# Performance work log

Hardware: AMD Instinct MI355X
Metric: run time of the kernel (lower is better)

Reference implementation:

```python
import jax, jax.numpy as jnp
import numpy as np

# --- quantization-format simulation helpers (numpy, used only in setup) ---
FP4_GRID = np.array([0.0, 0.5, 1.0, 1.5, 2.0, 3.0, 4.0, 6.0], np.float32)  # e2m1 magnitudes
FP4_MID = (FP4_GRID[:-1] + FP4_GRID[1:]) / 2.0
E4M3_MAX = 448.0


def _round_e4m3(x):
    """Round-to-nearest onto an fp8 e4m3-like grid (3 mantissa bits, clamp to 448)."""
    x = np.clip(x, -E4M3_MAX, E4M3_MAX)
    a = np.abs(x)
    e = np.clip(np.floor(np.log2(np.maximum(a, 1e-12))), -6, 8)
    step = np.exp2(e - 3)
    return (np.round(x / step) * step).astype(np.float32)


def _quant_fp4_mag(a):
    """Nearest e2m1 magnitude for non-negative a."""
    idx = np.searchsorted(FP4_MID, a)
    return FP4_GRID[idx]


def setup_inputs() -> dict:
    rng = np.random.default_rng(0)
    IN, OUT, P = 4096, 4096, 8
    k_fp8 = ((IN // P + 127) // 128) * 128   # 512
    k_fp4 = IN - k_fp8                       # 3584

    w = (rng.standard_normal((OUT, IN)) * 0.023).astype(np.float32)
    w4 = w[:, :k_fp4]
    w8 = w[:, k_fp4:]

    # --- NVFP4 quantization: per-128 fp32 outer scale, per-16 e4m3 inner scale ---
    b128 = w4.reshape(OUT, k_fp4 // 128, 128)
    os = np.maximum(np.abs(b128).max(-1) / (6.0 * E4M3_MAX), 1e-12).astype(np.float32)  # (OUT, k4/128)
    b16 = w4.reshape(OUT, k_fp4 // 128, 8, 16)
    is_q = _round_e4m3(np.abs(b16).max(-1) / 6.0 / os[..., None])  # (OUT, k4/128, 8)
    denom = np.maximum(is_q * os[..., None], 1e-12)
    q4 = np.sign(b16) * _quant_fp4_mag(np.abs(b16) / denom[..., None])
    w_q_fp4 = q4.reshape(OUT, k_fp4).astype(np.float32)
    w_is_fp4 = is_q.reshape(OUT, k_fp4 // 16).astype(np.float32)
    w_os_fp4 = os

    # --- fp8 quantization: per-32 e8m0 (power-of-2) scale ---
    b32 = w8.reshape(OUT, k_fp8 // 32, 32)
    amax = np.maximum(np.abs(b32).max(-1), 1e-12)
    s8 = np.exp2(np.ceil(np.log2(amax / E4M3_MAX))).astype(np.float32)
    w_q_fp8 = _round_e4m3(b32 / s8[..., None]).reshape(OUT, k_fp8)
    w_s_fp8 = s8

    # --- dequantized transposed weight buffer (as the module precomputes) ---
    w4_dq = w_q_fp4 * np.repeat(w_is_fp4, 16, 1) * np.repeat(w_os_fp4, 128, 1)
    w8_dq = w_q_fp8 * np.repeat(w_s_fp8, 32, 1)
    w_t = np.ascontiguousarray(np.concatenate([w4_dq, w8_dq], 1).T)  # (IN, OUT)

    x = rng.standard_normal((8192, IN)).astype(np.float32)
    return {
        "x": jnp.asarray(x),
        "w_q_fp4": jnp.asarray(w_q_fp4),
        "w_os_fp4": jnp.asarray(w_os_fp4),
        "w_is_fp4": jnp.asarray(w_is_fp4),
        "w_t": jnp.asarray(w_t),
        "w_q_fp8": jnp.asarray(w_q_fp8),
        "w_s_fp8": jnp.asarray(w_s_fp8),
    }


def reference(x, w_q_fp4, w_os_fp4, w_is_fp4, w_t, w_q_fp8, w_s_fp8):
    OUT = w_q_fp4.shape[0]
    k4 = w_q_fp4.shape[1]
    # fused dequant of fp4 partition: value * inner_scale(per 16) * outer_scale(per 128)
    w4 = (w_q_fp4.reshape(OUT, k4 // 16, 16) * w_is_fp4[..., None]).reshape(OUT, k4)
    w4 = (w4.reshape(OUT, k4 // 128, 128) * w_os_fp4[..., None]).reshape(OUT, k4)
    # dequant of fp8 partition: value * e8m0 scale (per 32)
    k8 = w_q_fp8.shape[1]
    w8 = (w_q_fp8.reshape(OUT, k8 // 32, 32) * w_s_fp8[..., None]).reshape(OUT, k8)
    W = jnp.concatenate([w4, w8], axis=1)  # (OUT, IN)
    return x @ W.T  # (tokens, OUT)
```

## Files before the change

### kernel.cpp

```cpp
#include <hip/hip_runtime.h>
#include <stdint.h>

#define K_DIM 4096
#define N_DIM 4096
#define KS_DIM (K_DIM / 32)
#define NT_DIM (N_DIM / 16)

typedef __attribute__((ext_vector_type(8))) short s16x8;
typedef __attribute__((ext_vector_type(4))) float f32x4;

static __device__ __forceinline__ unsigned short f32_to_bf16(float f) {
    union { float f; unsigned int u; } v; v.f = f;
    unsigned int u = v.u;
    u += 0x7FFFu + ((u >> 16) & 1u);
    return (unsigned short)(u >> 16);
}


extern "C" __global__ void pack_x_k(const float* __restrict__ in,
                                    unsigned short* __restrict__ out, int MT) {
    int wid = blockIdx.x * 4 + (threadIdx.x >> 6);
    int lane = threadIdx.x & 63;
    int mt = wid % MT, ks = wid / MT;
    int r = lane & 15, q = lane >> 4;
    const float* src = in + (size_t)(mt * 16 + r) * K_DIM + ks * 32 + q * 8;
    float4 a = *(const float4*)src;
    float4 b = *(const float4*)(src + 4);
    s16x8 o;
    o[0] = (short)f32_to_bf16(a.x); o[1] = (short)f32_to_bf16(a.y);
    o[2] = (short)f32_to_bf16(a.z); o[3] = (short)f32_to_bf16(a.w);
    o[4] = (short)f32_to_bf16(b.x); o[5] = (short)f32_to_bf16(b.y);
    o[6] = (short)f32_to_bf16(b.z); o[7] = (short)f32_to_bf16(b.w);
    *(s16x8*)(out + ((size_t)wid * 64 + lane) * 8) = o;
}

extern "C" __global__ void pack_w_k(const float* __restrict__ in,
                                    unsigned short* __restrict__ out) {
    __shared__ __align__(16) unsigned short tile[64][72];
    int n0 = blockIdx.x * 64, k0 = blockIdx.y * 64;
    int t = threadIdx.x;
    int tr = t >> 4, tc = (t & 15) * 4;
#pragma unroll
    for (int i = 0; i < 4; ++i) {
        int k = tr + i * 16;
        float4 v = *(const float4*)(in + (size_t)(k0 + k) * N_DIM + n0 + tc);
        tile[tc + 0][k] = f32_to_bf16(v.x);
        tile[tc + 1][k] = f32_to_bf16(v.y);
        tile[tc + 2][k] = f32_to_bf16(v.z);
        tile[tc + 3][k] = f32_to_bf16(v.w);
    }
    __syncthreads();
    int f = t >> 5, h = f >> 2, ntl = f & 3;
    int ks = blockIdx.y * 2 + h;
    int nt = blockIdx.x * 4 + ntl;
    unsigned short* dst = out + ((size_t)(ks * NT_DIM + nt) * 64) * 8;
#pragma unroll
    for (int u = 0; u < 2; ++u) {
        int c = (t & 31) * 2 + u;
        int r = c & 15, q = c >> 4;
        s16x8 o = *(const s16x8*)&tile[ntl * 16 + r][h * 32 + q * 8];
        *(s16x8*)(dst + (size_t)c * 8) = o;
    }
}

__device__ __forceinline__ void async_cp16(const unsigned short* g, unsigned short* l) {
    __builtin_amdgcn_global_load_lds(
        (const __attribute__((address_space(1))) unsigned int*)g,
        (__attribute__((address_space(3))) unsigned int*)l, 16, 0, 0);
}

#define SLOTS 4
#define SLOT_SHORTS (32 * 512)

__device__ __forceinline__ void sbar() {
    __builtin_amdgcn_sched_barrier(0);
    __builtin_amdgcn_s_barrier();
    __builtin_amdgcn_sched_barrier(0);
}

template <int VM>
__device__ __forceinline__ void wait_vm() {
    if constexpr (VM == 8)      asm volatile("s_waitcnt vmcnt(8)" ::: "memory");
    else if constexpr (VM == 4) asm volatile("s_waitcnt vmcnt(4)" ::: "memory");
    else                        asm volatile("s_waitcnt vmcnt(0)" ::: "memory");
    __builtin_amdgcn_sched_barrier(0);
}

#define BODY(T, VM, STAGE)                                                  \
  {                                                                         \
    wait_vm<VM>();                                                          \
    sbar();                                                                 \
    if (STAGE) {                                                            \
      unsigned short* d = lds + (((T) + 3) & 3) * SLOT_SHORTS + dsOff;      \
      _Pragma("unroll")                                                     \
      for (int fi = 0; fi < 4; ++fi)                                        \
        async_cp16(gstage + fi * 512, d + fi * 512);                        \
      gstage += strideS;                                                    \
    }                                                                       \
    const unsigned short* a = lds + ((T) & 3) * SLOT_SHORTS + aOff;         \
    const unsigned short* b = lds + ((T) & 3) * SLOT_SHORTS + bOff;         \
    s16x8 af[8], bf[4];                                                     \
    _Pragma("unroll")                                                       \
    for (int i = 0; i < 8; ++i) af[i] = *(const s16x8*)(a + i * 512);       \
    _Pragma("unroll")                                                       \
    for (int j = 0; j < 4; ++j) bf[j] = *(const s16x8*)(b + j * 512);       \
    __builtin_amdgcn_s_setprio(1);                                          \
    _Pragma("unroll")                                                       \
    for (int i = 0; i < 8; ++i)                                             \
      _Pragma("unroll")                                                     \
      for (int j = 0; j < 4; ++j)                                           \
        acc[i][j] = __builtin_amdgcn_mfma_f32_16x16x32_bf16(                \
            af[i], bf[j], acc[i][j], 0, 0, 0);                              \
    __builtin_amdgcn_s_setprio(0);                                          \
  }

extern "C" __global__ __launch_bounds__(512, 2)
void gemm_pk(const unsigned short* __restrict__ Ap,
             const unsigned short* __restrict__ Bp,
             float* __restrict__ C, int M) {
    __shared__ __align__(16) unsigned short lds[SLOTS * SLOT_SHORTS];
    const int MT = M >> 4;
    const int tid = threadIdx.x;
    const int wave = tid >> 6, lane = tid & 63;

    const int nwg = gridDim.x;
    const int cpx = nwg >> 3;
    const int swz = (blockIdx.x & 7) * cpx + (blockIdx.x >> 3);
    const int bn = swz & (N_DIM / 256 - 1);
    const int bm = swz >> 4;

    const int wm2 = wave >> 2;
    const int wn4 = wave & 3;
    const int fr0 = (wave & 3) * 4;

    const unsigned short* gstage = wm2
        ? Bp + (((size_t)bn * 16 + fr0) * 64 + lane) * 8
        : Ap + (((size_t)bm * 16 + fr0) * 64 + lane) * 8;
    const size_t strideS = (size_t)(wm2 ? NT_DIM : MT) * 512;
    const int dsOff = (wm2 * 16 + fr0) * 512;

    const int aOff = (wm2 * 8) * 512 + lane * 8;
    const int bOff = (16 + wn4 * 4) * 512 + lane * 8;

    f32x4 acc[8][4] = {};

#pragma unroll
    for (int t = 0; t < SLOTS - 1; ++t) {
        unsigned short* d = lds + t * SLOT_SHORTS + dsOff;
#pragma unroll
        for (int fi = 0; fi < 4; ++fi)
            async_cp16(gstage + fi * 512, d + fi * 512);
        gstage += strideS;
    }

    for (int t = 0; t < KS_DIM - 2; ++t)
        BODY(t, 8, (t + 3 < KS_DIM));
    BODY(KS_DIM - 2, 4, false);
    BODY(KS_DIM - 1, 0, false);

    const size_t tileM = (size_t)bm * 256, tileN = (size_t)bn * 256;
#pragma unroll
    for (int i = 0; i < 8; ++i)
#pragma unroll
        for (int j = 0; j < 4; ++j) {
            size_t row = tileM + wm2 * 128 + i * 16 + (lane >> 4) * 4;
            size_t col = tileN + wn4 * 64 + j * 16 + (lane & 15);
#pragma unroll
            for (int r = 0; r < 4; ++r)
                C[(row + r) * N_DIM + col] = acc[i][j][r];
        }
}

extern "C" __global__ __launch_bounds__(256)
void gemm_f32_k(const float* __restrict__ X,
                const float* __restrict__ Wt,
                float* __restrict__ C, int M) {
    const int K = K_DIM, N = N_DIM;
    __shared__ __align__(16) unsigned short sA[128 * 32];
    __shared__ __align__(16) unsigned short sB[128 * 32];
    const int tid = threadIdx.x;
    const int wave = tid >> 6, lane = tid & 63;
    const int wm = (wave >> 1) * 64, wn = (wave & 1) * 64;
    const size_t tileM = (size_t)blockIdx.y * 128, tileN = (size_t)blockIdx.x * 128;
    const int frow = lane & 15, fcol = (lane >> 4) * 8;
    f32x4 acc[4][4] = {};
    for (int k0 = 0; k0 < K; k0 += 32) {
        __syncthreads();
#pragma unroll
        for (int it = 0; it < 4; ++it) {
            int idx = it * 256 + tid;
            int m = idx >> 3, c4 = (idx & 7) * 4;
            float4 v = *(const float4*)(X + (tileM + m) * (size_t)K + k0 + c4);
            sA[m * 32 + c4 + 0] = f32_to_bf16(v.x);
            sA[m * 32 + c4 + 1] = f32_to_bf16(v.y);
            sA[m * 32 + c4 + 2] = f32_to_bf16(v.z);
            sA[m * 32 + c4 + 3] = f32_to_bf16(v.w);
        }
#pragma unroll
        for (int it = 0; it < 16; ++it) {
            int idx = it * 256 + tid;
            int k = idx >> 7, n = idx & 127;
            float v = Wt[(size_t)(k0 + k) * N + tileN + n];
            sB[n * 32 + k] = f32_to_bf16(v);
        }
        __syncthreads();
        s16x8 af[4], bfr[4];
#pragma unroll
        for (int i = 0; i < 4; ++i)
            af[i] = *(const s16x8*)(sA + (wm + i * 16 + frow) * 32 + fcol);
#pragma unroll
        for (int j = 0; j < 4; ++j)
            bfr[j] = *(const s16x8*)(sB + (wn + j * 16 + frow) * 32 + fcol);
#pragma unroll
        for (int i = 0; i < 4; ++i)
#pragma unroll
            for (int j = 0; j < 4; ++j)
                acc[i][j] = __builtin_amdgcn_mfma_f32_16x16x32_bf16(
                    af[i], bfr[j], acc[i][j], 0, 0, 0);
    }
#pragma unroll
    for (int i = 0; i < 4; ++i)
#pragma unroll
        for (int j = 0; j < 4; ++j) {
            size_t row = tileM + wm + i * 16 + (lane >> 4) * 4;
            size_t col = tileN + wn + j * 16 + (lane & 15);
#pragma unroll
            for (int r = 0; r < 4; ++r)
                C[(row + r) * N + col] = acc[i][j][r];
        }
}

extern "C" void kernel_launch(void* const* d_in, const int* in_sizes, int n_in,
                              void* d_out, int out_size, void* d_ws, size_t ws_size,
                              hipStream_t stream) {
    const float* x   = (const float*)d_in[0];
    const float* w_t = (const float*)d_in[4];
    float* out = (float*)d_out;
    const int K = K_DIM, N = N_DIM;
    const int M = in_sizes[0] / K;
    const int MT = M / 16;
    const size_t need = (size_t)M * K * 2 + (size_t)N * K * 2;
    if (ws_size >= need && (M % 256) == 0) {
        unsigned short* ap = (unsigned short*)d_ws;
        unsigned short* bp = ap + (size_t)M * K;
        int nwave = KS_DIM * MT;
        hipLaunchKernelGGL(pack_x_k, dim3(nwave / 4), dim3(256), 0, stream,
                           x, ap, MT);
        hipLaunchKernelGGL(pack_w_k, dim3(N / 64, K / 64), dim3(256), 0, stream,
                           w_t, bp);
        hipLaunchKernelGGL(gemm_pk, dim3((M / 256) * (N / 256)), dim3(512), 0,
                           stream, ap, bp, out, M);
    } else {
        hipLaunchKernelGGL(gemm_f32_k, dim3(N / 128, M / 128), dim3(256), 0, stream,
                           x, w_t, out, M);
    }
}
```

Before: 533.4 us.

## Split GEMM k-step into two half-phases and stage pack_x through LDS

The main GEMM loop now splits each k-step into two halves. Each half loads four A fragments, issues half of the async global-to-LDS copies, then runs its MFMA group, so LDS reads, global prefetch and matrix math interleave with the barrier moved after the fragment loads. The vmcnt wait moves to the second half, and the prologue and epilogue are reworked to match. Separately, pack_x_k now reads contiguous 1024-wide row chunks into an LDS tile and writes the packed fragment layout from there, aiming for coalesced global reads. The cost is an extra barrier per k-step and more delicate wait-count bookkeeping, which could expose hazards in the slot reuse.

```diff
diff --git a/kernel.cpp b/kernel.cpp
--- a/kernel.cpp
+++ b/kernel.cpp
@@ -17,21 +17,32 @@
 }
 
 
-extern "C" __global__ void pack_x_k(const float* __restrict__ in,
-                                    unsigned short* __restrict__ out, int MT) {
-    int wid = blockIdx.x * 4 + (threadIdx.x >> 6);
-    int lane = threadIdx.x & 63;
-    int mt = wid % MT, ks = wid / MT;
-    int r = lane & 15, q = lane >> 4;
-    const float* src = in + (size_t)(mt * 16 + r) * K_DIM + ks * 32 + q * 8;
-    float4 a = *(const float4*)src;
-    float4 b = *(const float4*)(src + 4);
-    s16x8 o;
-    o[0] = (short)f32_to_bf16(a.x); o[1] = (short)f32_to_bf16(a.y);
-    o[2] = (short)f32_to_bf16(a.z); o[3] = (short)f32_to_bf16(a.w);
-    o[4] = (short)f32_to_bf16(b.x); o[5] = (short)f32_to_bf16(b.y);
-    o[6] = (short)f32_to_bf16(b.z); o[7] = (short)f32_to_bf16(b.w);
-    *(s16x8*)(out + ((size_t)wid * 64 + lane) * 8) = o;
+extern "C" __global__ __launch_bounds__(256)
+void pack_x_k(const float* __restrict__ in,
+              unsigned short* __restrict__ out, int MT) {
+    __shared__ __align__(16) unsigned short tile[16][1032];
+    const int kc = blockIdx.x;
+    const int mt = blockIdx.y;
+    const int t = threadIdx.x;
+#pragma unroll
+    for (int r = 0; r < 16; ++r) {
+        float4 v = *(const float4*)(in + (size_t)(mt * 16 + r) * K_DIM
+                                    + kc * 1024 + t * 4);
+        tile[r][t * 4 + 0] = f32_to_bf16(v.x);
+        tile[r][t * 4 + 1] = f32_to_bf16(v.y);
+        tile[r][t * 4 + 2] = f32_to_bf16(v.z);
+        tile[r][t * 4 + 3] = f32_to_bf16(v.w);
+    }
+    __syncthreads();
+#pragma unroll
+    for (int i = 0; i < 8; ++i) {
+        int chunk = i * 256 + t;
+        int f = chunk >> 6, L = chunk & 63;
+        int r = L & 15, q = L >> 4;
+        s16x8 v = *(const s16x8*)&tile[r][f * 32 + q * 8];
+        int ks = kc * 32 + f;
+        *(s16x8*)(out + ((size_t)(ks * MT + mt) * 64 + L) * 8) = v;
+    }
 }
 
 extern "C" __global__ void pack_w_k(const float* __restrict__ in,
@@ -82,35 +93,59 @@
 __device__ __forceinline__ void wait_vm() {
     if constexpr (VM == 8)      asm volatile("s_waitcnt vmcnt(8)" ::: "memory");
     else if constexpr (VM == 4) asm volatile("s_waitcnt vmcnt(4)" ::: "memory");
-    else                        asm volatile("s_waitcnt vmcnt(0)" ::: "memory");
+    else if constexpr (VM == 0) asm volatile("s_waitcnt vmcnt(0)" ::: "memory");
+    if constexpr (VM >= 0) __builtin_amdgcn_sched_barrier(0);
+}
+
+__device__ __forceinline__ void lgkm0() {
+    asm volatile("s_waitcnt lgkmcnt(0)" ::: "memory");
     __builtin_amdgcn_sched_barrier(0);
 }
 
 #define BODY(T, VM, STAGE)                                                  \
   {                                                                         \
-    wait_vm<VM>();                                                          \
-    sbar();                                                                 \
-    if (STAGE) {                                                            \
-      unsigned short* d = lds + (((T) + 3) & 3) * SLOT_SHORTS + dsOff;      \
-      _Pragma("unroll")                                                     \
-      for (int fi = 0; fi < 4; ++fi)                                        \
-        async_cp16(gstage + fi * 512, d + fi * 512);                        \
-      gstage += strideS;                                                    \
-    }                                                                       \
     const unsigned short* a = lds + ((T) & 3) * SLOT_SHORTS + aOff;         \
     const unsigned short* b = lds + ((T) & 3) * SLOT_SHORTS + bOff;         \
-    s16x8 af[8], bf[4];                                                     \
-    _Pragma("unroll")                                                       \
-    for (int i = 0; i < 8; ++i) af[i] = *(const s16x8*)(a + i * 512);       \
+    unsigned short* d = lds + (((T) + 3) & 3) * SLOT_SHORTS + dsOff;        \
+                                                     \
+    s16x8 af[4], bf[4];                                                     \
+    _Pragma("unroll")                                                       \
+    for (int i = 0; i < 4; ++i) af[i] = *(const s16x8*)(a + i * 512);       \
     _Pragma("unroll")                                                       \
     for (int j = 0; j < 4; ++j) bf[j] = *(const s16x8*)(b + j * 512);       \
+    if (STAGE) {                                                            \
+      async_cp16(gstage + 0 * 512, d + 0 * 512);                            \
+      async_cp16(gstage + 1 * 512, d + 1 * 512);                            \
+    }                                                                       \
+    sbar();                                                                 \
+    lgkm0();                                                                \
     __builtin_amdgcn_s_setprio(1);                                          \
     _Pragma("unroll")                                                       \
-    for (int i = 0; i < 8; ++i)                                             \
+    for (int i = 0; i < 4; ++i)                                             \
       _Pragma("unroll")                                                     \
       for (int j = 0; j < 4; ++j)                                           \
         acc[i][j] = __builtin_amdgcn_mfma_f32_16x16x32_bf16(                \
             af[i], bf[j], acc[i][j], 0, 0, 0);                              \
+    __builtin_amdgcn_s_setprio(0);                                          \
+                                                     \
+    s16x8 ag[4];                                                            \
+    _Pragma("unroll")                                                       \
+    for (int i = 0; i < 4; ++i) ag[i] = *(const s16x8*)(a + (4 + i) * 512); \
+    if (STAGE) {                                                            \
+      async_cp16(gstage + 2 * 512, d + 2 * 512);                            \
+      async_cp16(gstage + 3 * 512, d + 3 * 512);                            \
+      gstage += strideS;                                                    \
+    }                                                                       \
+    wait_vm<VM>();                                                          \
+    sbar();                                                                 \
+    lgkm0();                                                                \
+    __builtin_amdgcn_s_setprio(1);                                          \
+    _Pragma("unroll")                                                       \
+    for (int i = 0; i < 4; ++i)                                             \
+      _Pragma("unroll")                                                     \
+      for (int j = 0; j < 4; ++j)                                           \
+        acc[4 + i][j] = __builtin_amdgcn_mfma_f32_16x16x32_bf16(            \
+            ag[i], bf[j], acc[4 + i][j], 0, 0, 0);                          \
     __builtin_amdgcn_s_setprio(0);                                          \
   }
 
@@ -152,11 +187,14 @@
             async_cp16(gstage + fi * 512, d + fi * 512);
         gstage += strideS;
     }
-
-    for (int t = 0; t < KS_DIM - 2; ++t)
-        BODY(t, 8, (t + 3 < KS_DIM));
-    BODY(KS_DIM - 2, 4, false);
-    BODY(KS_DIM - 1, 0, false);
+    wait_vm<8>();
+    sbar();
+
+    for (int t = 0; t < KS_DIM - 3; ++t)
+        BODY(t, 8, true);
+    BODY(KS_DIM - 3, 4, false);
+    BODY(KS_DIM - 2, 0, false);
+    BODY(KS_DIM - 1, -1, false);
 
     const size_t tileM = (size_t)bm * 256, tileN = (size_t)bn * 256;
 #pragma unroll
@@ -243,8 +281,7 @@
     if (ws_size >= need && (M % 256) == 0) {
         unsigned short* ap = (unsigned short*)d_ws;
         unsigned short* bp = ap + (size_t)M * K;
-        int nwave = KS_DIM * MT;
-        hipLaunchKernelGGL(pack_x_k, dim3(nwave / 4), dim3(256), 0, stream,
+        hipLaunchKernelGGL(pack_x_k, dim3(K / 1024, M / 16), dim3(256), 0, stream,
                            x, ap, MT);
         hipLaunchKernelGGL(pack_w_k, dim3(N / 64, K / 64), dim3(256), 0, stream,
                            w_t, bp);
```

Result: faster. 517.4 us (-3.0%).
